# Kernel optimization log

Measured on AMD Instinct MI355X. Metric: run time of the kernel, lower is better.

## Reference

```python
import jax, jax.numpy as jnp
import numpy as np

LOG2PI = float(np.log(2.0 * np.pi))
BATCH = 131072
IN_FEATURES = 128
MULT = 3          # Gaussian multiplicity / Sum in_channels
CARD = 2          # first Product cardinality -> 64 features


def setup_inputs() -> dict:
    key = jax.random.key(0)
    k1, k2, k3, k4, k5 = jax.random.split(key, 5)
    x = jax.random.normal(k1, (BATCH, IN_FEATURES), dtype=jnp.float32)
    means = jax.random.normal(k2, (1, IN_FEATURES, MULT), dtype=jnp.float32)
    # stds drawn positive (torch.rand init for scale params)
    stds = jax.random.uniform(k3, (1, IN_FEATURES, MULT), dtype=jnp.float32,
                              minval=0.1, maxval=1.0)
    sum_weights = jax.random.normal(k4, (64, MULT, 1), dtype=jnp.float32)
    # randomized Product layer: fixed random permutation of the 128 features
    perm = jax.random.permutation(k5, IN_FEATURES).astype(jnp.int32)
    return {"x": x, "means": means, "stds": stds,
            "sum_weights": sum_weights, "perm": perm}


def reference(x, means, stds, sum_weights, perm):
    n = x.shape[0]
    # --- Gaussian leaf: Normal(mu, sigma).log_prob(x) -> [n, 128, 3]
    z = (x[:, :, None] - means) / stds
    lp = -0.5 * (z * z) - jnp.log(stds) - 0.5 * LOG2PI
    # --- Product(in_features=128, cardinality=2, randomize): permute features,
    # pair them up, product in log-domain = sum -> [n, 64, 3]
    lp = lp[:, perm, :]
    lp = lp.reshape(n, IN_FEATURES // CARD, CARD, MULT).sum(axis=2)
    # --- Sum(in_channels=3, in_features=64, out_channels=1): weighted
    # log-sum-exp mixture over channels with log_softmax-normalized weights
    logw = jax.nn.log_softmax(sum_weights, axis=1)          # [64, 3, 1]
    lp = jax.nn.logsumexp(lp[:, :, :, None] + logw[None], axis=2)  # [n, 64, 1]
    # --- Product(in_features=64, cardinality=64): sum all features -> [n, 1, 1]
    # (permutation before a full reduction is a no-op, so omitted)
    out = lp.sum(axis=1, keepdims=True).reshape(n, 1, 1)
    return out
```

## Files before the change

### kernel.cpp

```cpp
#include <hip/hip_runtime.h>

#define N_FEAT 128
#define ROWS   32
#define TPB    256
#define GRID   1024

#define WAITV(N) asm volatile("s_waitcnt vmcnt(" #N ")" ::: "memory")

template<int CTRL>
__device__ __forceinline__ float dpp_xadd(float v) {
    int t = __builtin_amdgcn_update_dpp(0, __float_as_int(v), CTRL, 0xF, 0xF, true);
    return v + __int_as_float(t);
}

__device__ __forceinline__ float wave_allsum(float v) {
    v = dpp_xadd<0xB1>(v);
    v = dpp_xadd<0x4E>(v);
    v = dpp_xadd<0x141>(v);
    v = dpp_xadd<0x140>(v);
#if __has_builtin(__builtin_amdgcn_permlane16_swap)
    {
        auto p = __builtin_amdgcn_permlane16_swap(__float_as_uint(v), __float_as_uint(v), false, false);
        v = __uint_as_float(p[0]) + __uint_as_float(p[1]);
    }
#else
    v += __int_as_float(__builtin_amdgcn_ds_swizzle(__float_as_int(v), 0x401F));
#endif
    {
        auto p = __builtin_amdgcn_permlane32_swap(__float_as_uint(v), __float_as_uint(v), false, false);
        v = __uint_as_float(p[0]) + __uint_as_float(p[1]);
    }
    return v;
}

__global__ __launch_bounds__(TPB, 4)
void spn_fused(const float* __restrict__ x,
               const float* __restrict__ means,
               const float* __restrict__ stds,
               const float* __restrict__ sumw,
               const int* __restrict__ perm,
               float* __restrict__ out, int n) {
    __shared__ float sx[2 * ROWS * N_FEAT];

    const float NHALF_LOG2E = -0.7213475204444817f;
    const float LN2      = 0.6931471805599453f;
    const float LOG2E    = 1.4426950408889634f;
    const float L2PI_L2E = 2.6514961294723187f;

    const int tid  = threadIdx.x;
    const int lane = tid & 63;
    const int wv   = tid >> 6;

    float* buf0 = sx + wv * (8 * N_FEAT);
    float* buf1 = sx + 4 * (8 * N_FEAT) + wv * (8 * N_FEAT);

    const int ntiles = n / ROWS;
    const int stride = gridDim.x;

    auto issue = [&](int t, float* dst) {
        const float* g0 = x + (size_t)t * (ROWS * N_FEAT) + wv * (8 * N_FEAT);
#pragma unroll
        for (int it = 0; it < 4; ++it) {
            __builtin_amdgcn_global_load_lds(
                (const __attribute__((address_space(1))) unsigned*)(g0 + it * 256 + lane * 4),
                (__attribute__((address_space(3))) unsigned*)(dst + it * 256),
                16, 0, 0);
        }
    };

    const int t0 = blockIdx.x;
    if (t0 < ntiles) issue(t0, buf0);

    const int g  = lane;
    const int p0 = perm[2 * g], p1 = perm[2 * g + 1];
    float w2[3];
#pragma unroll
    for (int m = 0; m < 3; ++m) w2[m] = sumw[g * 3 + m] * LOG2E;
    const float mx2 = fmaxf(w2[0], fmaxf(w2[1], w2[2]));
    const float lse2 = mx2 + __builtin_amdgcn_logf(__builtin_amdgcn_exp2f(w2[0] - mx2)
                                                 + __builtin_amdgcn_exp2f(w2[1] - mx2)
                                                 + __builtin_amdgcn_exp2f(w2[2] - mx2));
    float nm0[3], is0[3], nm1[3], is1[3], C2[3];
#pragma unroll
    for (int m = 0; m < 3; ++m) {
        const float s0 = stds[p0 * 3 + m], mu0 = means[p0 * 3 + m];
        const float s1 = stds[p1 * 3 + m], mu1 = means[p1 * 3 + m];
        const float i0 = 1.0f / s0, i1 = 1.0f / s1;
        nm0[m] = mu0 * i0;  is0[m] = i0;
        nm1[m] = mu1 * i1;  is1[m] = i1;
        C2[m]  = (w2[m] - lse2) - __builtin_amdgcn_logf(s0)
                                - __builtin_amdgcn_logf(s1) - L2PI_L2E;
    }

    WAITV(0);

    int k = 0;
    for (int t = t0; t < ntiles; t += stride, ++k) {
        float* cbuf = (k & 1) ? buf1 : buf0;
        const int tn = t + stride;
        if (tn < ntiles) {
            issue(tn, (k & 1) ? buf0 : buf1);
            WAITV(6);
        } else {
            WAITV(2);
        }

        float res[8];
#pragma unroll
        for (int r = 0; r < 8; ++r) {
            const float* xr = cbuf + r * N_FEAT;
            const float a = xr[p0];
            const float b = xr[p1];
            float v0, v1, v2;
            {
                float z0 = fmaf(a, is0[0], -nm0[0]);
                float z1 = fmaf(b, is1[0], -nm1[0]);
                v0 = fmaf(z0 * z0, NHALF_LOG2E, C2[0]);
                v0 = fmaf(z1 * z1, NHALF_LOG2E, v0);
            }
            {
                float z0 = fmaf(a, is0[1], -nm0[1]);
                float z1 = fmaf(b, is1[1], -nm1[1]);
                v1 = fmaf(z0 * z0, NHALF_LOG2E, C2[1]);
                v1 = fmaf(z1 * z1, NHALF_LOG2E, v1);
            }
            {
                float z0 = fmaf(a, is0[2], -nm0[2]);
                float z1 = fmaf(b, is1[2], -nm1[2]);
                v2 = fmaf(z0 * z0, NHALF_LOG2E, C2[2]);
                v2 = fmaf(z1 * z1, NHALF_LOG2E, v2);
            }
            float pmx = fmaxf(v0, fmaxf(v1, v2));
            float s = __builtin_amdgcn_exp2f(v0 - pmx)
                    + __builtin_amdgcn_exp2f(v1 - pmx)
                    + __builtin_amdgcn_exp2f(v2 - pmx);
            res[r] = pmx + __builtin_amdgcn_logf(s);
        }

#pragma unroll
        for (int r = 0; r < 8; ++r)
            res[r] = wave_allsum(res[r]);

        if (lane == 0) {
            float4* op = (float4*)(out + t * ROWS + wv * 8);
            op[0] = make_float4(res[0] * LN2, res[1] * LN2, res[2] * LN2, res[3] * LN2);
            op[1] = make_float4(res[4] * LN2, res[5] * LN2, res[6] * LN2, res[7] * LN2);
        }
    }
}

extern "C" void kernel_launch(void* const* d_in, const int* in_sizes, int n_in,
                              void* d_out, int out_size, void* d_ws, size_t ws_size,
                              hipStream_t stream) {
    const float* x     = (const float*)d_in[0];
    const float* means = (const float*)d_in[1];
    const float* stds  = (const float*)d_in[2];
    const float* sumw  = (const float*)d_in[3];
    const int*   perm  = (const int*)d_in[4];
    float* out = (float*)d_out;
    int n = in_sizes[0] / N_FEAT;

    int ntiles = n / ROWS;
    int grid = GRID < ntiles ? GRID : (ntiles > 0 ? ntiles : 1);

    hipLaunchKernelGGL(spn_fused, dim3(grid), dim3(TPB), 0, stream,
                       x, means, stds, sumw, perm, out, n);
}
```

Measured before the change: 99.82 us.

## Replace LDS async staging with direct permuted global gathers into registers

Drops the global_load_lds double-buffered shared-memory staging and the manual vmcnt waits. Each lane now gathers its two permuted features straight from global memory into registers, with a two-stage register double buffer for prefetch. This removes LDS traffic and the shared-memory footprint, which may raise occupancy. The cost is uncoalesced 4-byte scattered global loads in place of 16-byte contiguous ones, which lean on the cache to merge line accesses.

Result: slower. 102.0 us (+2.2%).

```diff
diff --git a/kernel.cpp b/kernel.cpp
--- a/kernel.cpp
+++ b/kernel.cpp
@@ -4,8 +4,6 @@
 #define ROWS   32
 #define TPB    256
 #define GRID   1024
-
-#define WAITV(N) asm volatile("s_waitcnt vmcnt(" #N ")" ::: "memory")
 
 template<int CTRL>
 __device__ __forceinline__ float dpp_xadd(float v) {
@@ -40,8 +38,6 @@
                const float* __restrict__ sumw,
                const int* __restrict__ perm,
                float* __restrict__ out, int n) {
-    __shared__ float sx[2 * ROWS * N_FEAT];
-
     const float NHALF_LOG2E = -0.7213475204444817f;
     const float LN2      = 0.6931471805599453f;
     const float LOG2E    = 1.4426950408889634f;
@@ -51,25 +47,8 @@
     const int lane = tid & 63;
     const int wv   = tid >> 6;
 
-    float* buf0 = sx + wv * (8 * N_FEAT);
-    float* buf1 = sx + 4 * (8 * N_FEAT) + wv * (8 * N_FEAT);
-
     const int ntiles = n / ROWS;
     const int stride = gridDim.x;
-
-    auto issue = [&](int t, float* dst) {
-        const float* g0 = x + (size_t)t * (ROWS * N_FEAT) + wv * (8 * N_FEAT);
-#pragma unroll
-        for (int it = 0; it < 4; ++it) {
-            __builtin_amdgcn_global_load_lds(
-                (const __attribute__((address_space(1))) unsigned*)(g0 + it * 256 + lane * 4),
-                (__attribute__((address_space(3))) unsigned*)(dst + it * 256),
-                16, 0, 0);
-        }
-    };
-
-    const int t0 = blockIdx.x;
-    if (t0 < ntiles) issue(t0, buf0);
 
     const int g  = lane;
     const int p0 = perm[2 * g], p1 = perm[2 * g + 1];
@@ -92,25 +71,23 @@
                                 - __builtin_amdgcn_logf(s1) - L2PI_L2E;
     }
 
-    WAITV(0);
+    const float* xw = x + (size_t)wv * (8 * N_FEAT);
 
-    int k = 0;
-    for (int t = t0; t < ntiles; t += stride, ++k) {
-        float* cbuf = (k & 1) ? buf1 : buf0;
-        const int tn = t + stride;
-        if (tn < ntiles) {
-            issue(tn, (k & 1) ? buf0 : buf1);
-            WAITV(6);
-        } else {
-            WAITV(2);
+    auto load_tile = [&](int t, float* A, float* B) {
+        const float* base = xw + (size_t)t * (ROWS * N_FEAT);
+#pragma unroll
+        for (int r = 0; r < 8; ++r) {
+            A[r] = base[r * N_FEAT + p0];
+            B[r] = base[r * N_FEAT + p1];
         }
+    };
 
+    auto compute_store = [&](const float* A, const float* B, int t) {
         float res[8];
 #pragma unroll
         for (int r = 0; r < 8; ++r) {
-            const float* xr = cbuf + r * N_FEAT;
-            const float a = xr[p0];
-            const float b = xr[p1];
+            const float a = A[r];
+            const float b = B[r];
             float v0, v1, v2;
             {
                 float z0 = fmaf(a, is0[0], -nm0[0]);
@@ -146,6 +123,24 @@
             op[0] = make_float4(res[0] * LN2, res[1] * LN2, res[2] * LN2, res[3] * LN2);
             op[1] = make_float4(res[4] * LN2, res[5] * LN2, res[6] * LN2, res[7] * LN2);
         }
+    };
+
+    int t = blockIdx.x;
+    if (t >= ntiles) return;
+
+    float aA[8], bA[8], aB[8], bB[8];
+    load_tile(t, aA, bA);
+    while (true) {
+        const int t1 = t + stride;
+        if (t1 < ntiles) load_tile(t1, aB, bB);
+        compute_store(aA, bA, t);
+        if (t1 >= ntiles) break;
+
+        const int t2 = t1 + stride;
+        if (t2 < ntiles) load_tile(t2, aA, bA);
+        compute_store(aB, bB, t1);
+        if (t2 >= ntiles) break;
+        t = t2;
     }
 }
 
```
